# Performance work log

Hardware: AMD Instinct MI355X
Metric: run time of the kernel (lower is better)

The kernel has to match this reference:

```python
import jax, jax.numpy as jnp
import numpy as np

N = 50000        # nodes
F = 128          # input feature dim
U = 128          # units (output dim)
E_RAND = 1_600_000  # random edges; N self-loops appended -> E = 1_650_000
LABEL_IDXS = np.array([0, 5, 17, 42], dtype=np.int32)  # label_idxs init arg (indices into F)


def setup_inputs() -> dict:
    key = jax.random.key(0)
    k1, k2, k3, k4, k5 = jax.random.split(key, 5)
    x = jax.random.normal(k1, (1, N, F), dtype=jnp.float32)
    src = jax.random.randint(k2, (E_RAND,), 0, N, dtype=jnp.int32)
    dst = jax.random.randint(k3, (E_RAND,), 0, N, dtype=jnp.int32)
    # append self-loops so the diagonal of A (Adiag term) is nontrivial,
    # matching a normalized Laplacian which always has diagonal entries
    loops = jnp.arange(N, dtype=jnp.int32)
    edge_src = jnp.concatenate([src, loops])
    edge_dst = jnp.concatenate([dst, loops])
    edge_w = jax.random.uniform(k4, (E_RAND + N,), dtype=jnp.float32)
    kernel = jax.random.normal(k5, (F, U), dtype=jnp.float32) * (1.0 / np.sqrt(F))
    bias = jnp.zeros((U,), dtype=jnp.float32)
    return {"x": x, "edge_src": edge_src, "edge_dst": edge_dst,
            "edge_w": edge_w, "kernel": kernel, "bias": bias}


def reference(x, edge_src, edge_dst, edge_w, kernel, bias):
    # x: [1, N, F]; sparse A given as COO edges (edge_src=row i, edge_dst=col j, edge_w=A[i,j])
    n = x.shape[1]
    xs = x[0]  # [N, F]
    # A @ X  (sparse matmul via gather + segment_sum)
    agg = jax.ops.segment_sum(edge_w[:, None] * xs[edge_dst], edge_src, num_segments=n)  # [N, F]
    # diag(A): entries where row == col
    diag = jax.ops.segment_sum(jnp.where(edge_src == edge_dst, edge_w, jnp.float32(0.0)),
                               edge_src, num_segments=n)  # [N]
    # B = sum_{i in label_idxs} e_i e_i^T is a diagonal 0/1 selector on feature columns,
    # so (Adiag @ X) @ B == diag[:,None] * (X * mask)
    mask = jnp.zeros((xs.shape[1],), xs.dtype).at[jnp.asarray(LABEL_IDXS)].set(1.0)  # [F]
    h = agg - diag[:, None] * (xs * mask)  # [N, F]
    out = jax.nn.relu(h @ kernel + bias)   # [N, U]
    return out[None]  # [1, N, U]
```

## Files before the change

### kernel.cpp

```cpp
#include <hip/hip_runtime.h>

#define FDIM 128
#define UDIM 128
#define BROWS 256
#define CAP   9728
#define TILE  4096
#define EPT   16

typedef __attribute__((ext_vector_type(8))) short short8;
typedef __attribute__((ext_vector_type(4))) float floatx4;

__device__ inline unsigned int round_bf16_bits(float a) {
  unsigned int ua = __float_as_uint(a);
  ua += 0x7fffu + ((ua >> 16) & 1u);
  return ua & 0xffff0000u;
}
__device__ inline unsigned int pack_bf16(float a, float b) {
  unsigned int ua = __float_as_uint(a);
  unsigned int ub = __float_as_uint(b);
  ua += 0x7fffu + ((ua >> 16) & 1u);
  ub += 0x7fffu + ((ub >> 16) & 1u);
  return (ua >> 16) | (ub & 0xffff0000u);
}

__global__ __launch_bounds__(256) void bin_edges(
    const int* __restrict__ src, const int* __restrict__ dst,
    const float* __restrict__ w, int* __restrict__ cursor,
    unsigned int* __restrict__ binned_dstw, unsigned char* __restrict__ binned_src,
    float* __restrict__ diag, int E, int NB) {
  __shared__ int scnt[256];
  __shared__ int sbase[256];
  __shared__ int scur[256];
  int t = threadIdx.x;
  scnt[t] = 0; scur[t] = 0;
  __syncthreads();

  uint2 pay[EPT];
  int e0 = blockIdx.x * TILE;
  #pragma unroll
  for (int j = 0; j < EPT; ++j) {
    int e = e0 + j * 256 + t;
    if (e < E) {
      int s = src[e];
      int d = dst[e];
      float wv = w[e];
      if (s == d) atomicAdd(&diag[s], wv);
      pay[j].x = round_bf16_bits(wv) | (unsigned int)d;
      pay[j].y = (unsigned int)s;
      atomicAdd(&scnt[s >> 8], 1);
    } else {
      pay[j].y = 0xffffffffu;
    }
  }
  __syncthreads();

  if (t < NB) {
    int c = scnt[t];
    if (c) sbase[t] = t * CAP + atomicAdd(&cursor[t], c);
  }
  __syncthreads();

  #pragma unroll
  for (int j = 0; j < EPT; ++j) {
    if (pay[j].y != 0xffffffffu) {
      int b = pay[j].y >> 8;
      int r = atomicAdd(&scur[b], 1);
      int pos = sbase[b] + r;
      if (pos < (b + 1) * CAP) {
        binned_dstw[pos] = pay[j].x;
        binned_src[pos] = (unsigned char)(pay[j].y & 255u);
      }
    }
  }
}

__global__ __launch_bounds__(256) void scan_buckets(
    const int* __restrict__ cursor, int* __restrict__ bucket_base,
    int* __restrict__ rs, int NB, int N) {
  __shared__ int s[256];
  int t = threadIdx.x;
  int local = 0;
  if (t < NB) {
    int c = cursor[t];
    local = (c > CAP) ? CAP : c;
  }
  s[t] = local; __syncthreads();
  int v = local;
  for (int off = 1; off < 256; off <<= 1) {
    int add = (t >= off) ? s[t - off] : 0;
    __syncthreads();
    v += add; s[t] = v;
    __syncthreads();
  }
  if (t < NB) bucket_base[t] = v - local;
  if (t == 255) rs[N] = s[255];
}

__global__ __launch_bounds__(256) void sort_bucket(
    const unsigned int* __restrict__ binned_dstw,
    const unsigned char* __restrict__ binned_src,
    const int* __restrict__ cursor, const int* __restrict__ bucket_base,
    int* __restrict__ rs, unsigned int* __restrict__ meta, int N) {
  __shared__ unsigned char ssrc[CAP];
  __shared__ int rcnt[256];
  int b = blockIdx.x;
  int t = threadIdx.x;
  int row0 = b * BROWS;
  int nrows = N - row0; if (nrows > BROWS) nrows = BROWS;
  int cntE = cursor[b]; if (cntE > CAP) cntE = CAP;
  int base_in = b * CAP;
  int base_out = bucket_base[b];

  rcnt[t] = 0;
  __syncthreads();
  for (int e = t; e < cntE; e += 256) {
    unsigned char sl = binned_src[base_in + e];
    ssrc[e] = sl;
    atomicAdd(&rcnt[sl], 1);
  }
  __syncthreads();

  int local = rcnt[t];
  int v = local;
  for (int off = 1; off < 256; off <<= 1) {
    int add = (t >= off) ? rcnt[t - off] : 0;
    __syncthreads();
    v += add; rcnt[t] = v;
    __syncthreads();
  }
  int cur0 = base_out + (v - local);
  if (t < nrows) rs[row0 + t] = cur0;
  rcnt[t] = cur0;
  __syncthreads();

  for (int e = t; e < cntE; e += 256) {
    unsigned char sl = ssrc[e];
    int pos = atomicAdd(&rcnt[sl], 1);
    meta[pos] = binned_dstw[base_in + e];
  }
}

__global__ __launch_bounds__(64) void prep_kfrag(
    const float* __restrict__ K, uint4* __restrict__ kfrag) {
  int lane = threadIdx.x;
  int n = (blockIdx.x >> 2) * 16 + (lane & 15);
  int k0 = (blockIdx.x & 3) * 32 + (lane >> 4) * 8;
  unsigned int p[4];
  #pragma unroll
  for (int j = 0; j < 4; ++j) {
    float a = K[(size_t)(k0 + 2 * j) * UDIM + n];
    float b = K[(size_t)(k0 + 2 * j + 1) * UDIM + n];
    p[j] = pack_bf16(a, b);
  }
  kfrag[(size_t)blockIdx.x * 64 + lane] = make_uint4(p[0], p[1], p[2], p[3]);
}

__global__ __launch_bounds__(256) void gemm_y_mfma(
    const float* __restrict__ x, const uint4* __restrict__ kfrag,
    unsigned short* __restrict__ Ybf, int N) {
  __shared__ unsigned short sX[64][136];
  int t = threadIdx.x;
  int r0 = blockIdx.x * 64;

  #pragma unroll
  for (int i = 0; i < 8; ++i) {
    int li = i * 256 + t;
    int row = li >> 5;
    int col4 = (li & 31) * 4;
    int gr = r0 + row; if (gr > N - 1) gr = N - 1;
    float4 v = *(const float4*)(x + (size_t)gr * FDIM + col4);
    *(uint2*)(&sX[row][col4]) = make_uint2(pack_bf16(v.x, v.y), pack_bf16(v.z, v.w));
  }
  __syncthreads();

  int wave = t >> 6, lane = t & 63;
  int m = lane & 15, q = lane >> 4;

  short8 bf[2][4];
  #pragma unroll
  for (int c = 0; c < 2; ++c)
    #pragma unroll
    for (int ks = 0; ks < 4; ++ks)
      bf[c][ks] = *(const short8*)&kfrag[(size_t)((2 * wave + c) * 4 + ks) * 64 + lane];

  floatx4 acc[4][2];
  #pragma unroll
  for (int rt = 0; rt < 4; ++rt)
    #pragma unroll
    for (int c = 0; c < 2; ++c)
      acc[rt][c] = (floatx4){0.f, 0.f, 0.f, 0.f};

  #pragma unroll
  for (int ks = 0; ks < 4; ++ks) {
    #pragma unroll
    for (int rt = 0; rt < 4; ++rt) {
      short8 af = *(const short8*)&sX[rt * 16 + m][ks * 32 + q * 8];
      acc[rt][0] = __builtin_amdgcn_mfma_f32_16x16x32_bf16(af, bf[0][ks], acc[rt][0], 0, 0, 0);
      acc[rt][1] = __builtin_amdgcn_mfma_f32_16x16x32_bf16(af, bf[1][ks], acc[rt][1], 0, 0, 0);
    }
  }

  #pragma unroll
  for (int rt = 0; rt < 4; ++rt) {
    #pragma unroll
    for (int c = 0; c < 2; ++c) {
      int col = (2 * wave + c) * 16 + m;
      #pragma unroll
      for (int reg = 0; reg < 4; ++reg) {
        int r = r0 + rt * 16 + q * 4 + reg;
        if (r < N)
          Ybf[(size_t)r * UDIM + col] =
              (unsigned short)(round_bf16_bits(acc[rt][c][reg]) >> 16);
      }
    }
  }
}

__global__ __launch_bounds__(256) void gather_out(
    const unsigned short* __restrict__ Ybf, const int* __restrict__ rs,
    const unsigned int* __restrict__ meta,
    const float* __restrict__ diag, const float* __restrict__ x,
    const float* __restrict__ K, const float* __restrict__ bias,
    float* __restrict__ out, int N) {
  int r = blockIdx.x * 8 + (threadIdx.x >> 5);
  if (r >= N) return;
  int sub = threadIdx.x & 31;
  int base = rs[r], end = rs[r + 1];
  int len = end - base;

  unsigned int m0 = 0, m1 = 0;
  if (sub < len) m0 = __builtin_nontemporal_load(&meta[base + sub]);
  if (32 + sub < len) m1 = __builtin_nontemporal_load(&meta[base + 32 + sub]);

  float4 acc = {0.f, 0.f, 0.f, 0.f};
  int nk = len < 64 ? len : 64;
  int i = 0;
  for (; i + 8 <= nk; i += 8) {
    unsigned int msel = (i & 32) ? m1 : m0;
    unsigned int mi[8];
    #pragma unroll
    for (int j = 0; j < 8; ++j) mi[j] = __shfl(msel, (i + j) & 31, 32);
    uint2 pk[8];
    #pragma unroll
    for (int j = 0; j < 8; ++j)
      pk[j] = *(const uint2*)(Ybf + (size_t)(mi[j] & 0xffffu) * UDIM + sub * 4);
    #pragma unroll
    for (int j = 0; j < 8; ++j) {
      float wj = __uint_as_float(mi[j] & 0xffff0000u);
      acc.x += wj * __uint_as_float(pk[j].x << 16);
      acc.y += wj * __uint_as_float(pk[j].x & 0xffff0000u);
      acc.z += wj * __uint_as_float(pk[j].y << 16);
      acc.w += wj * __uint_as_float(pk[j].y & 0xffff0000u);
    }
  }
  for (; i < nk; ++i) {
    unsigned int mi = __shfl((i & 32) ? m1 : m0, i & 31, 32);
    float wj = __uint_as_float(mi & 0xffff0000u);
    uint2 pk = *(const uint2*)(Ybf + (size_t)(mi & 0xffffu) * UDIM + sub * 4);
    acc.x += wj * __uint_as_float(pk.x << 16);
    acc.y += wj * __uint_as_float(pk.x & 0xffff0000u);
    acc.z += wj * __uint_as_float(pk.y << 16);
    acc.w += wj * __uint_as_float(pk.y & 0xffff0000u);
  }
  for (int k0 = base + 64; k0 < end; k0 += 32) {
    int nk2 = end - k0; if (nk2 > 32) nk2 = 32;
    unsigned int m2 = 0;
    if (sub < nk2) m2 = __builtin_nontemporal_load(&meta[k0 + sub]);
    for (int j = 0; j < nk2; ++j) {
      unsigned int mi = __shfl(m2, j, 32);
      float wj = __uint_as_float(mi & 0xffff0000u);
      uint2 pk = *(const uint2*)(Ybf + (size_t)(mi & 0xffffu) * UDIM + sub * 4);
      acc.x += wj * __uint_as_float(pk.x << 16);
      acc.y += wj * __uint_as_float(pk.x & 0xffff0000u);
      acc.z += wj * __uint_as_float(pk.y << 16);
      acc.w += wj * __uint_as_float(pk.y & 0xffff0000u);
    }
  }

  float dg = diag[r];
  const int lf[4] = {0, 5, 17, 42};
  #pragma unroll
  for (int tt = 0; tt < 4; ++tt) {
    float c = dg * x[(size_t)r * FDIM + lf[tt]];
    float4 k4 = *(const float4*)(K + lf[tt] * UDIM + sub * 4);
    acc.x -= c * k4.x; acc.y -= c * k4.y;
    acc.z -= c * k4.z; acc.w -= c * k4.w;
  }

  float4 b4 = *(const float4*)(bias + sub * 4);
  acc.x = fmaxf(acc.x + b4.x, 0.f);
  acc.y = fmaxf(acc.y + b4.y, 0.f);
  acc.z = fmaxf(acc.z + b4.z, 0.f);
  acc.w = fmaxf(acc.w + b4.w, 0.f);
  *(float4*)(out + (size_t)r * UDIM + sub * 4) = acc;
}

extern "C" void kernel_launch(void* const* d_in, const int* in_sizes, int n_in,
                              void* d_out, int out_size, void* d_ws, size_t ws_size,
                              hipStream_t stream) {
  const float* x    = (const float*)d_in[0];
  const int*   esrc = (const int*)d_in[1];
  const int*   edst = (const int*)d_in[2];
  const float* ew   = (const float*)d_in[3];
  const float* K    = (const float*)d_in[4];
  const float* bias = (const float*)d_in[5];
  float* out = (float*)d_out;

  const int N = in_sizes[0] / FDIM;
  const int E = in_sizes[1];
  const int NB = (N + BROWS - 1) / BROWS;

  char* p = (char*)d_ws;
  unsigned short* Ybf = (unsigned short*)p; p += (size_t)N * UDIM * 2;
  float* diag  = (float*)p;         p += (size_t)N * 4;
  int*   cursor = (int*)p;          p += (size_t)NB * 4;
  int*   rs    = (int*)p;           p += (size_t)(N + 1) * 4;
  int*   bbase  = (int*)p;          p += (size_t)NB * 4;
  uint4* kfrag = (uint4*)p;         p += (size_t)32 * 64 * 16;
  unsigned int* binned_dstw = (unsigned int*)p; p += (size_t)NB * CAP * 4;
  unsigned int* meta = (unsigned int*)p;        p += (size_t)E * 4;
  unsigned char* binned_src = (unsigned char*)p; p += (size_t)NB * CAP;

  hipMemsetAsync(diag, 0, (size_t)(N + NB) * 4, stream);

  prep_kfrag<<<32, 64, 0, stream>>>(K, kfrag);
  bin_edges<<<(E + TILE - 1) / TILE, 256, 0, stream>>>(
      esrc, edst, ew, cursor, binned_dstw, binned_src, diag, E, NB);
  scan_buckets<<<1, 256, 0, stream>>>(cursor, bbase, rs, NB, N);
  sort_bucket<<<NB, 256, 0, stream>>>(binned_dstw, binned_src, cursor, bbase,
                                      rs, meta, N);

  gemm_y_mfma<<<(N + 63) / 64, 256, 0, stream>>>(x, kfrag, Ybf, N);
  gather_out<<<(N + 7) / 8, 256, 0, stream>>>(Ybf, rs, meta, diag, x, K, bias, out, N);
}
```

Baseline: 209.8 us.

## Fold bucket scan into sort kernel and sub-sort edges by destination quarter

After: 207.8 us. No clear change (-1.0%).

```diff
diff --git a/kernel.cpp b/kernel.cpp
--- a/kernel.cpp
+++ b/kernel.cpp
@@ -74,68 +74,69 @@
   }
 }
 
-__global__ __launch_bounds__(256) void scan_buckets(
-    const int* __restrict__ cursor, int* __restrict__ bucket_base,
-    int* __restrict__ rs, int NB, int N) {
-  __shared__ int s[256];
-  int t = threadIdx.x;
-  int local = 0;
-  if (t < NB) {
-    int c = cursor[t];
-    local = (c > CAP) ? CAP : c;
-  }
-  s[t] = local; __syncthreads();
-  int v = local;
-  for (int off = 1; off < 256; off <<= 1) {
-    int add = (t >= off) ? s[t - off] : 0;
-    __syncthreads();
-    v += add; s[t] = v;
-    __syncthreads();
-  }
-  if (t < NB) bucket_base[t] = v - local;
-  if (t == 255) rs[N] = s[255];
-}
-
 __global__ __launch_bounds__(256) void sort_bucket(
     const unsigned int* __restrict__ binned_dstw,
     const unsigned char* __restrict__ binned_src,
-    const int* __restrict__ cursor, const int* __restrict__ bucket_base,
-    int* __restrict__ rs, unsigned int* __restrict__ meta, int N) {
-  __shared__ unsigned char ssrc[CAP];
-  __shared__ int rcnt[256];
+    const int* __restrict__ cursor,
+    int* __restrict__ rs, unsigned int* __restrict__ meta, int N, int NB) {
+  __shared__ unsigned short skey[CAP];
+  __shared__ int kcnt[1024];
+  __shared__ int pscan[256];
   int b = blockIdx.x;
   int t = threadIdx.x;
   int row0 = b * BROWS;
   int nrows = N - row0; if (nrows > BROWS) nrows = BROWS;
+  int base_in = b * CAP;
+
+  int cb = 0;
+  if (t < NB) { cb = cursor[t]; if (cb > CAP) cb = CAP; }
+  pscan[t] = cb;
+  __syncthreads();
+  int v = cb;
+  for (int off = 1; off < 256; off <<= 1) {
+    int add = (t >= off) ? pscan[t - off] : 0;
+    __syncthreads();
+    v += add; pscan[t] = v;
+    __syncthreads();
+  }
   int cntE = cursor[b]; if (cntE > CAP) cntE = CAP;
-  int base_in = b * CAP;
-  int base_out = bucket_base[b];
-
-  rcnt[t] = 0;
-  __syncthreads();
+  int base_out = pscan[b] - cntE;
+  if (b == 0 && t == 0) rs[N] = pscan[NB - 1];
+
+  kcnt[t] = 0; kcnt[256 + t] = 0; kcnt[512 + t] = 0; kcnt[768 + t] = 0;
+  __syncthreads();
+
   for (int e = t; e < cntE; e += 256) {
-    unsigned char sl = binned_src[base_in + e];
-    ssrc[e] = sl;
-    atomicAdd(&rcnt[sl], 1);
-  }
-  __syncthreads();
-
-  int local = rcnt[t];
-  int v = local;
+    unsigned int dw = binned_dstw[base_in + e];
+    int sl = binned_src[base_in + e];
+    int key = (sl << 2) | (int)(((dw & 0xffffu) * 41u) >> 19);
+    skey[e] = (unsigned short)key;
+    atomicAdd(&kcnt[key], 1);
+  }
+  __syncthreads();
+
+  int c0 = kcnt[4 * t], c1 = kcnt[4 * t + 1], c2 = kcnt[4 * t + 2], c3 = kcnt[4 * t + 3];
+  int local = c0 + c1 + c2 + c3;
+  pscan[t] = local;
+  __syncthreads();
+  int v2 = local;
   for (int off = 1; off < 256; off <<= 1) {
-    int add = (t >= off) ? rcnt[t - off] : 0;
+    int add = (t >= off) ? pscan[t - off] : 0;
     __syncthreads();
-    v += add; rcnt[t] = v;
+    v2 += add; pscan[t] = v2;
     __syncthreads();
   }
-  int cur0 = base_out + (v - local);
-  if (t < nrows) rs[row0 + t] = cur0;
-  rcnt[t] = cur0;
+  int excl = base_out + v2 - local;
+  if (t < nrows) rs[row0 + t] = excl;
+  kcnt[4 * t] = excl;
+  kcnt[4 * t + 1] = excl + c0;
+  kcnt[4 * t + 2] = excl + c0 + c1;
+  kcnt[4 * t + 3] = excl + c0 + c1 + c2;
   __syncthreads();
 
   for (int e = t; e < cntE; e += 256) {
-    unsigned char sl = ssrc[e];
-    int pos = atomicAdd(&rcnt[sl], 1);
+    int key = skey[e];
+    int pos = atomicAdd(&kcnt[key], 1);
     meta[pos] = binned_dstw[base_in + e];
   }
 }
@@ -315,7 +316,6 @@
   float* diag  = (float*)p;         p += (size_t)N * 4;
   int*   cursor = (int*)p;          p += (size_t)NB * 4;
   int*   rs    = (int*)p;           p += (size_t)(N + 1) * 4;
-  int*   bbase  = (int*)p;          p += (size_t)NB * 4;
   uint4* kfrag = (uint4*)p;         p += (size_t)32 * 64 * 16;
   unsigned int* binned_dstw = (unsigned int*)p; p += (size_t)NB * CAP * 4;
   unsigned int* meta = (unsigned int*)p;        p += (size_t)E * 4;
@@ -326,9 +326,8 @@
   prep_kfrag<<<32, 64, 0, stream>>>(K, kfrag);
   bin_edges<<<(E + TILE - 1) / TILE, 256, 0, stream>>>(
       esrc, edst, ew, cursor, binned_dstw, binned_src, diag, E, NB);
-  scan_buckets<<<1, 256, 0, stream>>>(cursor, bbase, rs, NB, N);
-  sort_bucket<<<NB, 256, 0, stream>>>(binned_dstw, binned_src, cursor, bbase,
-                                      rs, meta, N);
+  sort_bucket<<<NB, 256, 0, stream>>>(binned_dstw, binned_src, cursor,
+                                      rs, meta, N, NB);
 
   gemm_y_mfma<<<(N + 63) / 64, 256, 0, stream>>>(x, kfrag, Ybf, N);
   gather_out<<<(N + 7) / 8, 256, 0, stream>>>(Ybf, rs, meta, diag, x, K, bias, out, N);
```
